# Performance work log

Hardware: AMD Instinct MI355X
Metric: run time of the kernel (lower is better)

The kernel has to match this reference:

```python
import jax, jax.numpy as jnp
import numpy as np

# ----- static layer configuration (mirrors __init__ / _precompute_cg_tensor) -----
NODE_LS = [0, 0, 1, 1]          # node_l_values (multiplicity expressed via repetition; node_multiplicity=1)
EDGE_SH = 1                      # edge_sh_degree
H_LS = NODE_LS + NODE_LS + [0]   # l-values of h = [f_src, f_tgt, d]
H_DIMS = [2 * l + 1 for l in H_LS]
H_OFF = np.concatenate([[0], np.cumsum(H_DIMS)])
A_DIMS = [2 * l + 1 for l in range(EDGE_SH + 1)]
A_OFF = np.concatenate([[0], np.cumsum(A_DIMS)])
O_DIMS = [2 * l + 1 for l in NODE_LS]
O_OFF = np.concatenate([[0], np.cumsum(O_DIMS)])
F_DIM = int(O_OFF[-1])           # 8
A_DIM = int(A_OFF[-1])           # 4
N_NODES, N_EDGES = 100000, 1600000
MLP_DIMS = [2 * len(NODE_LS) + 1, 64, 32, len(NODE_LS)]  # 9 -> 64 -> 32 -> 4

def _levi_civita():
    e = np.zeros((3, 3, 3), np.float32)
    e[0, 1, 2] = e[1, 2, 0] = e[2, 0, 1] = 1.0
    e[0, 2, 1] = e[2, 1, 0] = e[1, 0, 2] = -1.0
    return e

# real SO(3) Clebsch-Gordan tensors (e3nn wigner_3j normalization: full contraction norm 1)
_CG = {
    (0, 0, 0): np.ones((1, 1, 1), np.float32),
    (0, 1, 1): (np.eye(3, dtype=np.float32) / np.sqrt(3.0)).reshape(1, 3, 3),
    (1, 0, 1): (np.eye(3, dtype=np.float32) / np.sqrt(3.0)).reshape(3, 1, 3),
    (1, 1, 0): (np.eye(3, dtype=np.float32) / np.sqrt(3.0)).reshape(3, 3, 1),
    (1, 1, 1): _levi_civita() / np.sqrt(6.0),
}

CONNECTIONS = []  # (h_idx, a_l, out_idx, cg[h,a,o]) -- same enumeration order as the torch loop
for _h_idx, _hl in enumerate(H_LS):
    for _al in range(EDGE_SH + 1):
        for _oi, _ol in enumerate(NODE_LS):
            if abs(_hl - _al) <= _ol <= _hl + _al and (_hl, _al, _ol) in _CG:
                CONNECTIONS.append((_h_idx, _al, _oi, jnp.asarray(_CG[(_hl, _al, _ol)])))


def _invariants(x):
    # s_i = [f_{l=0}, ||f_{l=1}||, ...] per l-slot (multiplicity 1)
    outs = []
    for i, l in enumerate(NODE_LS):
        s, e = int(O_OFF[i]), int(O_OFF[i + 1])
        if l == 0:
            outs.append(x[:, s:e])
        else:
            outs.append(jnp.linalg.norm(x[:, s:e], axis=1, keepdims=True))
    return jnp.concatenate(outs, axis=1)


def setup_inputs() -> dict:
    ks = jax.random.split(jax.random.key(0), 10)
    edge_index = jax.random.randint(ks[0], (2, N_EDGES), 0, N_NODES)
    f = jax.random.normal(ks[1], (N_NODES, F_DIM), jnp.float32)
    d = jax.random.uniform(ks[2], (N_EDGES, 1), jnp.float32)
    a = jax.random.normal(ks[3], (N_EDGES, A_DIM), jnp.float32)
    w1 = jax.random.normal(ks[4], (EDGE_SH + 1,), jnp.float32) * 0.1
    w2 = jax.random.normal(ks[5], (EDGE_SH + 1,), jnp.float32) * 0.1
    W0 = jax.random.normal(ks[6], (MLP_DIMS[0], MLP_DIMS[1]), jnp.float32) / np.sqrt(MLP_DIMS[0])
    b0 = jnp.zeros((MLP_DIMS[1],), jnp.float32)
    W1 = jax.random.normal(ks[7], (MLP_DIMS[1], MLP_DIMS[2]), jnp.float32) / np.sqrt(MLP_DIMS[1])
    b1 = jnp.zeros((MLP_DIMS[2],), jnp.float32)
    W2 = jax.random.normal(ks[8], (MLP_DIMS[2], MLP_DIMS[3]), jnp.float32) / np.sqrt(MLP_DIMS[2])
    b2 = jnp.zeros((MLP_DIMS[3],), jnp.float32)
    return {"edge_index": edge_index, "f": f, "d": d, "a": a, "w1": w1, "w2": w2,
            "W0": W0, "b0": b0, "W1": W1, "b1": b1, "W2": W2, "b2": b2}


def reference(edge_index, f, d, a, w1, w2, W0, b0, W1, b1, W2, b2):
    src, tgt = edge_index[0], edge_index[1]
    n = f.shape[0]
    h = jnp.concatenate([f[src], f[tgt], d], axis=1)  # [E, 17]
    messages = jnp.zeros((h.shape[0], F_DIM), f.dtype)
    for h_idx, a_l, out_idx, cg in CONNECTIONS:
        hs, he = int(H_OFF[h_idx]), int(H_OFF[h_idx + 1])
        as_, ae = int(A_OFF[a_l]), int(A_OFF[a_l + 1])
        os_, oe = int(O_OFF[out_idx]), int(O_OFF[out_idx + 1])
        raw = jnp.einsum('hao,eh,ea->eo', cg, h[:, hs:he], a[:, as_:ae])  # [E, 2*out_l+1]
        msg = jnp.tanh(w2[a_l] * jnp.tanh(w1[a_l] * raw))
        messages = messages.at[:, os_:oe].add(msg)
    agg = jax.ops.segment_sum(messages, tgt, num_segments=n)          # [N, 8]
    dist_sum = jax.ops.segment_sum(d, tgt, num_segments=n)           # [N, 1]
    counts = jax.ops.segment_sum(jnp.ones((h.shape[0],), f.dtype), tgt, num_segments=n)
    avg_d = dist_sum / (counts[:, None] + 1e-8)
    psi_in = jnp.concatenate([_invariants(f), _invariants(agg), avg_d], axis=1)  # [N, 9]
    x = jax.nn.relu(psi_in @ W0 + b0)
    x = jax.nn.relu(x @ W1 + b1)
    gates = jax.nn.sigmoid(x @ W2 + b2)  # [N, 4]
    gate_full = jnp.concatenate(
        [jnp.repeat(gates[:, i:i + 1], O_DIMS[i], axis=1) for i in range(len(NODE_LS))], axis=1)
    return f + gate_full * agg
```

## Files before the change

### kernel.cpp

```cpp
#include <hip/hip_runtime.h>
#include <math.h>

#define IS3 0.57735026918962576f
#define IS6 0.40824829046386302f

#define SHIFT 11
#define BSZ   2048
#define CAP   36864u
#define MQ    4096.0f
#define IMQ   (1.0f/4096.0f)

typedef float v2f __attribute__((ext_vector_type(2)));

__device__ __forceinline__ float fastrcp(float x) { return __builtin_amdgcn_rcpf(x); }
__device__ __forceinline__ v2f mk2(float a, float b) { v2f r; r.x = a; r.y = b; return r; }

__device__ __forceinline__ v2f Tnl2(v2f x, v2f tw1, v2f w2) {
    v2f t = tw1 * x;
    v2f e;
    e.x = __expf(t.x);
    e.y = __expf(t.y);
    v2f ep = e + 1.0f;
    v2f r;
    r.x = fastrcp(ep.x);
    r.y = fastrcp(ep.y);
    v2f u = 1.0f - 2.0f * r;
    v2f z = w2 * u;
    v2f z2 = z * z;
    v2f p = z2 * 0.133333333f - 0.333333333f;
    return z * z2 * p + z;
}

__device__ __forceinline__ int q16(float x) {
    int v = (int)rintf(x * MQ);
    v = v >  32767 ?  32767 : v;
    v = v < -32768 ? -32768 : v;
    return v;
}

__global__ __launch_bounds__(1024, 8) void route_kernel(
    const int* __restrict__ ei, const float* __restrict__ f,
    const float* __restrict__ d, const float* __restrict__ a,
    const float* __restrict__ w1p, const float* __restrict__ w2p,
    unsigned* __restrict__ tails,
    unsigned* __restrict__ qmeta,
    uint2* __restrict__ qmsg,
    int E, int nbuk)
{
    __shared__ unsigned hcnt[64];
    __shared__ unsigned hoff[64];
    int tid = threadIdx.x;
    if (tid < 64) hcnt[tid] = 0;

    int e = blockIdx.x * 1024 + tid;
    bool valid = (e < E);

    float tw10 = 2.0f * w1p[0], tw11 = 2.0f * w1p[1];
    float w20 = w2p[0], w21 = w2p[1];

    int t = 0, s = 0;
    float4 sA = make_float4(0.f,0.f,0.f,0.f), sB = sA, tA = sA, tB = sA, av = sA;
    float de = 0.f;
    if (valid) {
        t = ei[E + e];
        s = ei[e];
        const float4* f4 = (const float4*)f;
        sA = f4[2*s]; sB = f4[2*s+1];
        tA = f4[2*t]; tB = f4[2*t+1];
        de = d[e];
        av = ((const float4*)a)[e];
    }

    __syncthreads();

    unsigned b = 0, lrank = 0;
    if (valid) {
        b = (((unsigned)t) >> SHIFT) & 63u;
        lrank = atomicAdd(&hcnt[b], 1u);
    }
    __syncthreads();

    unsigned basek = 0;
    if (tid < nbuk && hcnt[tid] != 0u)
        basek = atomicAdd(&tails[tid * 64], hcnt[tid]);

    unsigned dq = 0;
    uint2 pk = make_uint2(0u, 0u);
    if (valid) {
        float a0 = av.x, ax = av.y, ay = av.z, az = av.w;
        float axs = ax * IS3, ays = ay * IS3, azs = az * IS3;
        float a03 = a0 * IS3;

        v2f twSX = mk2(tw10, tw11), w2SX = mk2(w20, w21);
        v2f twXY = mk2(tw11, tw11), w2XY = mk2(w21, w21);
        v2f twCX = mk2(tw11, tw10), w2CX = mk2(w21, w20);
        v2f twDD = mk2(tw10, tw10), w2DD = mk2(w20, w20);

        v2f aSX = mk2(a0, axs);
        v2f aYZ = mk2(ays, azs);

        float sc[5] = { sA.x, sA.y, tA.x, tA.y, de };
        float vx[4] = { sA.z, sB.y, tA.z, tB.y };
        float vy[4] = { sA.w, sB.z, tA.w, tB.z };
        float vz[4] = { sB.x, sB.w, tB.x, tB.w };

        v2f mSX = mk2(0.f, 0.f);
        v2f mYZ = mk2(0.f, 0.f);
        float cz6[4];

        #pragma unroll
        for (int i = 0; i < 5; ++i) {
            mSX += Tnl2(sc[i] * aSX, twSX, w2SX);
            mYZ += Tnl2(sc[i] * aYZ, twXY, w2XY);
        }
        #pragma unroll
        for (int i = 0; i < 4; ++i) {
            float dva = vx[i]*ax + vy[i]*ay + vz[i]*az;
            mSX += Tnl2(mk2(dva * IS3, vx[i] * a03), twCX, w2CX);
            mYZ += Tnl2(mk2(vy[i] * a03, vz[i] * a03), twDD, w2DD);
            float cx = vy[i]*az - vz[i]*ay;
            float cy = vz[i]*ax - vx[i]*az;
            float cz = vx[i]*ay - vy[i]*ax;
            v2f exy = Tnl2(mk2(cx * IS6, cy * IS6), twXY, w2XY);
            mSX.y += exy.x;
            mYZ.x += exy.y;
            cz6[i] = cz * IS6;
        }
        v2f g1 = Tnl2(mk2(cz6[0], cz6[1]), twXY, w2XY);
        v2f g2 = Tnl2(mk2(cz6[2], cz6[3]), twXY, w2XY);
        mYZ.y += (g1.x + g1.y) + (g2.x + g2.y);

        unsigned dqi = (unsigned)(de * 2047.0f + 0.5f);
        dq = dqi > 2047u ? 2047u : dqi;
        int qS = q16(mSX.x), qX = q16(mSX.y), qY = q16(mYZ.x), qZ = q16(mYZ.y);
        pk.x = ((unsigned)(unsigned short)qS) | (((unsigned)(unsigned short)qX) << 16);
        pk.y = ((unsigned)(unsigned short)qY) | (((unsigned)(unsigned short)qZ) << 16);
    }

    if (tid < nbuk) hoff[tid] = basek;
    __syncthreads();

    if (valid) {
        unsigned pos = hoff[b] + lrank;
        if (pos < CAP) {
            size_t idx = (size_t)b * CAP + pos;
            qmeta[idx] = (((unsigned)(t & (BSZ - 1))) << 11) | dq;
            qmsg[idx]  = pk;
        }
    }
}

__global__ __launch_bounds__(1024) void bucket_kernel(
    const unsigned* __restrict__ tails, const unsigned* __restrict__ qmeta,
    const uint2* __restrict__ qmsg, unsigned* __restrict__ partial,
    int nbuk, int seg)
{
    __shared__ unsigned long long accSX[BSZ];
    __shared__ unsigned long long accYZ[BSZ];
    __shared__ unsigned accM[BSZ];
    int wg = blockIdx.x;
    int b = wg / seg, sgi = wg % seg;
    for (int i = threadIdx.x; i < BSZ; i += 1024) {
        accSX[i] = 0ull; accYZ[i] = 0ull; accM[i] = 0u;
    }
    __syncthreads();

    unsigned tail = tails[b * 64];
    if (tail > CAP) tail = CAP;
    unsigned lo = (unsigned)(((unsigned long long)tail * sgi) / seg);
    unsigned hi = (unsigned)(((unsigned long long)tail * (sgi + 1)) / seg);
    size_t base = (size_t)b * CAP;

    for (unsigned q = lo + threadIdx.x; q < hi; q += 1024) {
        unsigned meta = qmeta[base + q];
        uint2 m = qmsg[base + q];
        int local = (int)(meta >> 11);
        int qS = (int)(short)(m.x & 0xFFFFu);
        int qX = (int)(short)(m.x >> 16);
        int qY = (int)(short)(m.y & 0xFFFFu);
        int qZ = (int)(short)(m.y >> 16);
        unsigned long long vSX =
            (((unsigned long long)(unsigned)qX) << 32) | (unsigned)(qS + 65536);
        unsigned long long vYZ =
            (((unsigned long long)(unsigned)qZ) << 32) | (unsigned)(qY + 65536);
        atomicAdd(&accSX[local], vSX);
        atomicAdd(&accYZ[local], vYZ);
        atomicAdd(&accM[local], (1u << 20) | (meta & 2047u));
    }
    __syncthreads();

    unsigned* dst = partial + (size_t)wg * (BSZ * 5);
    for (int i = threadIdx.x; i < BSZ; i += 1024) {
        unsigned long long sx = accSX[i], yz = accYZ[i];
        dst[0*BSZ + i] = (unsigned)sx;
        dst[1*BSZ + i] = (unsigned)(sx >> 32);
        dst[2*BSZ + i] = (unsigned)yz;
        dst[3*BSZ + i] = (unsigned)(yz >> 32);
        dst[4*BSZ + i] = accM[i];
    }
}

__global__ __launch_bounds__(512) void mlp_kernel(
    const float* __restrict__ f, const unsigned* __restrict__ partial,
    const float* __restrict__ W0, const float* __restrict__ b0,
    const float* __restrict__ W1, const float* __restrict__ b1,
    const float* __restrict__ W2, const float* __restrict__ b2,
    float* __restrict__ out, int N, int seg)
{
    __shared__ float4 sW0t4[64*3];
    __shared__ float4 sW1v[64*8];
    __shared__ float4 sW2v[32];
    __shared__ float  sb0[64];
    __shared__ float4 sb1v[8];
    __shared__ float4 sb2v[1];

    int tid = threadIdx.x;
    float* w0t = (float*)sW0t4;
    for (int idx = tid; idx < 576; idx += 512) {
        int k = idx >> 6, i = idx & 63;
        w0t[i * 12 + k] = W0[idx];
    }
    if (tid < 192) {
        int i = tid / 3, k = 9 + tid % 3;
        w0t[i * 12 + k] = 0.f;
    }
    { float* p = (float*)sW1v; for (int idx = tid; idx < 2048; idx += 512) p[idx] = W1[idx]; }
    { float* p = (float*)sW2v; if (tid < 128) p[tid] = W2[tid]; }
    if (tid < 64) sb0[tid] = b0[tid];
    { float* p = (float*)sb1v; if (tid < 32) p[tid] = b1[tid]; }
    { float* p = (float*)sb2v; if (tid < 4)  p[tid] = b2[tid]; }
    __syncthreads();

    int n = blockIdx.x * 512 + tid;
    if (n >= N) return;

    int b = n >> SHIFT;
    int local = n & (BSZ - 1);
    int S = 0, X = 0, Y = 0, Z = 0, cnt = 0, dqs = 0;
    for (int s2 = 0; s2 < seg; ++s2) {
        const unsigned* p = partial + ((size_t)(b * seg + s2)) * (BSZ * 5);
        unsigned m4 = p[4*BSZ + local];
        int c = (int)(m4 >> 20);
        S += (int)p[0*BSZ + local] - (c << 16);
        X += (int)p[1*BSZ + local];
        Y += (int)p[2*BSZ + local] - (c << 16);
        Z += (int)p[3*BSZ + local];
        dqs += (int)(m4 & 0xFFFFFu);
        cnt += c;
    }
    float aS = (float)S * IMQ, ax = (float)X * IMQ;
    float ay = (float)Y * IMQ, az = (float)Z * IMQ;
    float cf = (float)cnt;
    float dsum = (float)dqs * (1.0f / 2047.0f);

    float4 fA = ((const float4*)f)[2*n];
    float4 fB = ((const float4*)f)[2*n+1];

    float nrm1 = sqrtf(fA.z*fA.z + fA.w*fA.w + fB.x*fB.x);
    float nrm2 = sqrtf(fB.y*fB.y + fB.z*fB.z + fB.w*fB.w);
    float nv   = sqrtf(ax*ax + ay*ay + az*az);
    float avgd = dsum * fastrcp(cf + 1e-8f);
    float4 p0 = make_float4(fA.x, fA.y, nrm1, nrm2);
    float4 p1 = make_float4(aS, aS, nv, nv);
    float4 p2 = make_float4(avgd, 0.f, 0.f, 0.f);

    float x1s[32];
    #pragma unroll
    for (int j = 0; j < 8; ++j) {
        float4 bv = sb1v[j];
        x1s[4*j+0] = bv.x; x1s[4*j+1] = bv.y; x1s[4*j+2] = bv.z; x1s[4*j+3] = bv.w;
    }
    #pragma unroll
    for (int i = 0; i < 64; ++i) {
        float4 r0 = sW0t4[i*3+0], r1 = sW0t4[i*3+1], r2 = sW0t4[i*3+2];
        float acc = sb0[i]
            + r0.x*p0.x + r0.y*p0.y + r0.z*p0.z + r0.w*p0.w
            + r1.x*p1.x + r1.y*p1.y + r1.z*p1.z + r1.w*p1.w
            + r2.x*p2.x;
        acc = fmaxf(acc, 0.f);
        #pragma unroll
        for (int j = 0; j < 8; ++j) {
            float4 wv = sW1v[i*8+j];
            x1s[4*j+0] += acc * wv.x;
            x1s[4*j+1] += acc * wv.y;
            x1s[4*j+2] += acc * wv.z;
            x1s[4*j+3] += acc * wv.w;
        }
    }
    #pragma unroll
    for (int j = 0; j < 32; ++j) x1s[j] = fmaxf(x1s[j], 0.f);

    float4 gb = sb2v[0];
    float g0 = gb.x, g1 = gb.y, g2 = gb.z, g3 = gb.w;
    #pragma unroll
    for (int i = 0; i < 32; ++i) {
        float4 wv = sW2v[i];
        g0 += x1s[i] * wv.x;
        g1 += x1s[i] * wv.y;
        g2 += x1s[i] * wv.z;
        g3 += x1s[i] * wv.w;
    }
    g0 = fastrcp(1.0f + __expf(-g0));
    g1 = fastrcp(1.0f + __expf(-g1));
    g2 = fastrcp(1.0f + __expf(-g2));
    g3 = fastrcp(1.0f + __expf(-g3));

    float* o = out + (size_t)8*n;
    o[0] = fA.x + g0*aS;
    o[1] = fA.y + g1*aS;
    o[2] = fA.z + g2*ax;
    o[3] = fA.w + g2*ay;
    o[4] = fB.x + g2*az;
    o[5] = fB.y + g3*ax;
    o[6] = fB.z + g3*ay;
    o[7] = fB.w + g3*az;
}

extern "C" void kernel_launch(void* const* d_in, const int* in_sizes, int n_in,
                              void* d_out, int out_size, void* d_ws, size_t ws_size,
                              hipStream_t stream) {
    const int*   ei = (const int*)d_in[0];
    const float* f  = (const float*)d_in[1];
    const float* d  = (const float*)d_in[2];
    const float* a  = (const float*)d_in[3];
    const float* w1 = (const float*)d_in[4];
    const float* w2 = (const float*)d_in[5];
    const float* W0 = (const float*)d_in[6];
    const float* b0 = (const float*)d_in[7];
    const float* W1 = (const float*)d_in[8];
    const float* b1 = (const float*)d_in[9];
    const float* W2 = (const float*)d_in[10];
    const float* b2 = (const float*)d_in[11];
    int E = in_sizes[0] / 2;
    int N = in_sizes[1] / 8;
    int nbuk = (N + BSZ - 1) >> SHIFT;

    size_t qn = (size_t)nbuk * CAP;
    size_t fixed = qn * 12 + (size_t)nbuk * 64 * 4;
    size_t per_seg = (size_t)nbuk * BSZ * 5 * 4;
    int segmax = nbuk > 0 ? (512 / nbuk) : 6;
    if (segmax < 1) segmax = 1;
    int seg = 6;
    if (ws_size > fixed + per_seg) {
        size_t m = (ws_size - fixed) / per_seg;
        seg = (int)(m < (size_t)segmax ? m : (size_t)segmax);
        if (seg < 1) seg = 1;
    }

    char* w = (char*)d_ws;
    uint2*    qmsg    = (uint2*)w;
    unsigned* qmeta   = (unsigned*)(w + qn * 8);
    unsigned* partial = (unsigned*)(w + qn * 12);
    unsigned* tails   = (unsigned*)(w + qn * 12 + (size_t)seg * per_seg);

    hipMemsetAsync(tails, 0, (size_t)nbuk * 64 * sizeof(unsigned), stream);

    int EB = (E + 1023) / 1024;
    route_kernel <<<dim3(EB), dim3(1024), 0, stream>>>(
        ei, f, d, a, w1, w2, tails, qmeta, qmsg, E, nbuk);
    bucket_kernel<<<dim3(nbuk * seg), dim3(1024), 0, stream>>>(
        tails, qmeta, qmsg, partial, nbuk, seg);
    mlp_kernel   <<<dim3((N + 511) / 512), dim3(512), 0, stream>>>(
        f, partial, W0, b0, W1, b1, W2, b2, (float*)d_out, N, seg);
}
```

Before: 175.0 us.

## Pre-pack MLP weights once and process two nodes per thread from global

Adds a one-block prep kernel that writes W0 (transposed and padded), W1, W2 and the biases into a packed workspace buffer. The MLP kernel then reads these uniform weights straight from global/scalar cache instead of staging them in shared memory with a barrier in every block. Each 64-thread block now handles two nodes per lane, so every weight load is reused across two rows. This costs one extra launch and doubles register pressure for the 32-wide hidden accumulators, which may lower occupancy.

```diff
diff --git a/kernel.cpp b/kernel.cpp
--- a/kernel.cpp
+++ b/kernel.cpp
@@ -9,6 +9,7 @@
 #define CAP   36864u
 #define MQ    4096.0f
 #define IMQ   (1.0f/4096.0f)
+#define WPAD  16384
 
 typedef float v2f __attribute__((ext_vector_type(2)));
 
@@ -36,6 +37,24 @@
     v = v >  32767 ?  32767 : v;
     v = v < -32768 ? -32768 : v;
     return v;
+}
+
+__global__ __launch_bounds__(1024) void prep_kernel(
+    const float* __restrict__ W0, const float* __restrict__ b0,
+    const float* __restrict__ W1, const float* __restrict__ b1,
+    const float* __restrict__ W2, const float* __restrict__ b2,
+    float* __restrict__ wp)
+{
+    int tid = threadIdx.x;
+    if (tid < 768) {
+        int i = tid / 12, k = tid % 12;
+        wp[tid] = (k < 9) ? W0[k * 64 + i] : 0.f;
+    }
+    for (int idx = tid; idx < 2048; idx += 1024) wp[768 + idx] = W1[idx];
+    if (tid < 128) wp[2816 + tid] = W2[tid];
+    if (tid < 64)  wp[2944 + tid] = b0[tid];
+    if (tid < 32)  wp[3008 + tid] = b1[tid];
+    if (tid < 4)   wp[3040 + tid] = b2[tid];
 }
 
 __global__ __launch_bounds__(1024, 8) void route_kernel(
@@ -200,120 +219,163 @@
     }
 }
 
-__global__ __launch_bounds__(512) void mlp_kernel(
+__global__ __launch_bounds__(64) void mlp_kernel(
     const float* __restrict__ f, const unsigned* __restrict__ partial,
-    const float* __restrict__ W0, const float* __restrict__ b0,
-    const float* __restrict__ W1, const float* __restrict__ b1,
-    const float* __restrict__ W2, const float* __restrict__ b2,
-    float* __restrict__ out, int N, int seg)
+    const float* __restrict__ wp, float* __restrict__ out, int N, int seg)
 {
-    __shared__ float4 sW0t4[64*3];
-    __shared__ float4 sW1v[64*8];
-    __shared__ float4 sW2v[32];
-    __shared__ float  sb0[64];
-    __shared__ float4 sb1v[8];
-    __shared__ float4 sb2v[1];
-
-    int tid = threadIdx.x;
-    float* w0t = (float*)sW0t4;
-    for (int idx = tid; idx < 576; idx += 512) {
-        int k = idx >> 6, i = idx & 63;
-        w0t[i * 12 + k] = W0[idx];
-    }
-    if (tid < 192) {
-        int i = tid / 3, k = 9 + tid % 3;
-        w0t[i * 12 + k] = 0.f;
-    }
-    { float* p = (float*)sW1v; for (int idx = tid; idx < 2048; idx += 512) p[idx] = W1[idx]; }
-    { float* p = (float*)sW2v; if (tid < 128) p[tid] = W2[tid]; }
-    if (tid < 64) sb0[tid] = b0[tid];
-    { float* p = (float*)sb1v; if (tid < 32) p[tid] = b1[tid]; }
-    { float* p = (float*)sb2v; if (tid < 4)  p[tid] = b2[tid]; }
-    __syncthreads();
-
-    int n = blockIdx.x * 512 + tid;
-    if (n >= N) return;
-
-    int b = n >> SHIFT;
-    int local = n & (BSZ - 1);
-    int S = 0, X = 0, Y = 0, Z = 0, cnt = 0, dqs = 0;
+    int lane = threadIdx.x;
+    int n0 = blockIdx.x * 128 + lane;
+    int n1 = n0 + 64;
+    if (n0 >= N) return;
+    bool vB = (n1 < N);
+
+    const float4* w0t4 = (const float4*)(wp);
+    const float4* w1v  = (const float4*)(wp + 768);
+    const float4* w2v  = (const float4*)(wp + 2816);
+    const float*  pb0  = wp + 2944;
+    const float4* b1v  = (const float4*)(wp + 3008);
+    const float4* b2v  = (const float4*)(wp + 3040);
+
+    int bA = n0 >> SHIFT, lA = n0 & (BSZ - 1);
+    int SA=0, XA=0, YA=0, ZA=0, cntA=0, dqsA=0;
     for (int s2 = 0; s2 < seg; ++s2) {
-        const unsigned* p = partial + ((size_t)(b * seg + s2)) * (BSZ * 5);
-        unsigned m4 = p[4*BSZ + local];
+        const unsigned* p = partial + ((size_t)(bA * seg + s2)) * (BSZ * 5);
+        unsigned m4 = p[4*BSZ + lA];
         int c = (int)(m4 >> 20);
-        S += (int)p[0*BSZ + local] - (c << 16);
-        X += (int)p[1*BSZ + local];
-        Y += (int)p[2*BSZ + local] - (c << 16);
-        Z += (int)p[3*BSZ + local];
-        dqs += (int)(m4 & 0xFFFFFu);
-        cnt += c;
-    }
-    float aS = (float)S * IMQ, ax = (float)X * IMQ;
-    float ay = (float)Y * IMQ, az = (float)Z * IMQ;
-    float cf = (float)cnt;
-    float dsum = (float)dqs * (1.0f / 2047.0f);
-
-    float4 fA = ((const float4*)f)[2*n];
-    float4 fB = ((const float4*)f)[2*n+1];
-
-    float nrm1 = sqrtf(fA.z*fA.z + fA.w*fA.w + fB.x*fB.x);
-    float nrm2 = sqrtf(fB.y*fB.y + fB.z*fB.z + fB.w*fB.w);
-    float nv   = sqrtf(ax*ax + ay*ay + az*az);
-    float avgd = dsum * fastrcp(cf + 1e-8f);
-    float4 p0 = make_float4(fA.x, fA.y, nrm1, nrm2);
-    float4 p1 = make_float4(aS, aS, nv, nv);
-    float4 p2 = make_float4(avgd, 0.f, 0.f, 0.f);
-
-    float x1s[32];
+        SA += (int)p[0*BSZ + lA] - (c << 16);
+        XA += (int)p[1*BSZ + lA];
+        YA += (int)p[2*BSZ + lA] - (c << 16);
+        ZA += (int)p[3*BSZ + lA];
+        dqsA += (int)(m4 & 0xFFFFFu);
+        cntA += c;
+    }
+    int bB = vB ? (n1 >> SHIFT) : 0, lB = vB ? (n1 & (BSZ - 1)) : 0;
+    int SB=0, XB=0, YB=0, ZB=0, cntB=0, dqsB=0;
+    if (vB) {
+        for (int s2 = 0; s2 < seg; ++s2) {
+            const unsigned* p = partial + ((size_t)(bB * seg + s2)) * (BSZ * 5);
+            unsigned m4 = p[4*BSZ + lB];
+            int c = (int)(m4 >> 20);
+            SB += (int)p[0*BSZ + lB] - (c << 16);
+            XB += (int)p[1*BSZ + lB];
+            YB += (int)p[2*BSZ + lB] - (c << 16);
+            ZB += (int)p[3*BSZ + lB];
+            dqsB += (int)(m4 & 0xFFFFFu);
+            cntB += c;
+        }
+    }
+
+    float aSA = (float)SA * IMQ, axA = (float)XA * IMQ;
+    float ayA = (float)YA * IMQ, azA = (float)ZA * IMQ;
+    float dsumA = (float)dqsA * (1.0f / 2047.0f);
+    float aSB = (float)SB * IMQ, axB = (float)XB * IMQ;
+    float ayB = (float)YB * IMQ, azB = (float)ZB * IMQ;
+    float dsumB = (float)dqsB * (1.0f / 2047.0f);
+
+    const float4* f4 = (const float4*)f;
+    float4 fA0 = f4[2*n0], fB0 = f4[2*n0+1];
+    float4 fA1 = make_float4(0.f,0.f,0.f,0.f), fB1 = fA1;
+    if (vB) { fA1 = f4[2*n1]; fB1 = f4[2*n1+1]; }
+
+    float nrm1A = sqrtf(fA0.z*fA0.z + fA0.w*fA0.w + fB0.x*fB0.x);
+    float nrm2A = sqrtf(fB0.y*fB0.y + fB0.z*fB0.z + fB0.w*fB0.w);
+    float nvA   = sqrtf(axA*axA + ayA*ayA + azA*azA);
+    float avgdA = dsumA * fastrcp((float)cntA + 1e-8f);
+    float4 p0A = make_float4(fA0.x, fA0.y, nrm1A, nrm2A);
+    float4 p1A = make_float4(aSA, aSA, nvA, nvA);
+
+    float nrm1B = sqrtf(fA1.z*fA1.z + fA1.w*fA1.w + fB1.x*fB1.x);
+    float nrm2B = sqrtf(fB1.y*fB1.y + fB1.z*fB1.z + fB1.w*fB1.w);
+    float nvB   = sqrtf(axB*axB + ayB*ayB + azB*azB);
+    float avgdB = dsumB * fastrcp((float)cntB + 1e-8f);
+    float4 p0B = make_float4(fA1.x, fA1.y, nrm1B, nrm2B);
+    float4 p1B = make_float4(aSB, aSB, nvB, nvB);
+
+    float x1A[32], x1B[32];
     #pragma unroll
     for (int j = 0; j < 8; ++j) {
-        float4 bv = sb1v[j];
-        x1s[4*j+0] = bv.x; x1s[4*j+1] = bv.y; x1s[4*j+2] = bv.z; x1s[4*j+3] = bv.w;
-    }
-    #pragma unroll
+        float4 bv = b1v[j];
+        x1A[4*j+0] = bv.x; x1A[4*j+1] = bv.y; x1A[4*j+2] = bv.z; x1A[4*j+3] = bv.w;
+        x1B[4*j+0] = bv.x; x1B[4*j+1] = bv.y; x1B[4*j+2] = bv.z; x1B[4*j+3] = bv.w;
+    }
+    #pragma unroll 8
     for (int i = 0; i < 64; ++i) {
-        float4 r0 = sW0t4[i*3+0], r1 = sW0t4[i*3+1], r2 = sW0t4[i*3+2];
-        float acc = sb0[i]
-            + r0.x*p0.x + r0.y*p0.y + r0.z*p0.z + r0.w*p0.w
-            + r1.x*p1.x + r1.y*p1.y + r1.z*p1.z + r1.w*p1.w
-            + r2.x*p2.x;
-        acc = fmaxf(acc, 0.f);
+        float4 r0 = w0t4[i*3+0], r1 = w0t4[i*3+1], r2 = w0t4[i*3+2];
+        float bb = pb0[i];
+        float accA = bb
+            + r0.x*p0A.x + r0.y*p0A.y + r0.z*p0A.z + r0.w*p0A.w
+            + r1.x*p1A.x + r1.y*p1A.y + r1.z*p1A.z + r1.w*p1A.w
+            + r2.x*avgdA;
+        float accB = bb
+            + r0.x*p0B.x + r0.y*p0B.y + r0.z*p0B.z + r0.w*p0B.w
+            + r1.x*p1B.x + r1.y*p1B.y + r1.z*p1B.z + r1.w*p1B.w
+            + r2.x*avgdB;
+        accA = fmaxf(accA, 0.f);
+        accB = fmaxf(accB, 0.f);
         #pragma unroll
         for (int j = 0; j < 8; ++j) {
-            float4 wv = sW1v[i*8+j];
-            x1s[4*j+0] += acc * wv.x;
-            x1s[4*j+1] += acc * wv.y;
-            x1s[4*j+2] += acc * wv.z;
-            x1s[4*j+3] += acc * wv.w;
+            float4 wv = w1v[i*8+j];
+            x1A[4*j+0] += accA * wv.x;
+            x1A[4*j+1] += accA * wv.y;
+            x1A[4*j+2] += accA * wv.z;
+            x1A[4*j+3] += accA * wv.w;
+            x1B[4*j+0] += accB * wv.x;
+            x1B[4*j+1] += accB * wv.y;
+            x1B[4*j+2] += accB * wv.z;
+            x1B[4*j+3] += accB * wv.w;
         }
     }
     #pragma unroll
-    for (int j = 0; j < 32; ++j) x1s[j] = fmaxf(x1s[j], 0.f);
-
-    float4 gb = sb2v[0];
-    float g0 = gb.x, g1 = gb.y, g2 = gb.z, g3 = gb.w;
+    for (int j = 0; j < 32; ++j) {
+        x1A[j] = fmaxf(x1A[j], 0.f);
+        x1B[j] = fmaxf(x1B[j], 0.f);
+    }
+
+    float4 gb = b2v[0];
+    float g0A = gb.x, g1A = gb.y, g2A = gb.z, g3A = gb.w;
+    float g0B = gb.x, g1B = gb.y, g2B = gb.z, g3B = gb.w;
     #pragma unroll
     for (int i = 0; i < 32; ++i) {
-        float4 wv = sW2v[i];
-        g0 += x1s[i] * wv.x;
-        g1 += x1s[i] * wv.y;
-        g2 += x1s[i] * wv.z;
-        g3 += x1s[i] * wv.w;
-    }
-    g0 = fastrcp(1.0f + __expf(-g0));
-    g1 = fastrcp(1.0f + __expf(-g1));
-    g2 = fastrcp(1.0f + __expf(-g2));
-    g3 = fastrcp(1.0f + __expf(-g3));
-
-    float* o = out + (size_t)8*n;
-    o[0] = fA.x + g0*aS;
-    o[1] = fA.y + g1*aS;
-    o[2] = fA.z + g2*ax;
-    o[3] = fA.w + g2*ay;
-    o[4] = fB.x + g2*az;
-    o[5] = fB.y + g3*ax;
-    o[6] = fB.z + g3*ay;
-    o[7] = fB.w + g3*az;
+        float4 wv = w2v[i];
+        g0A += x1A[i] * wv.x;
+        g1A += x1A[i] * wv.y;
+        g2A += x1A[i] * wv.z;
+        g3A += x1A[i] * wv.w;
+        g0B += x1B[i] * wv.x;
+        g1B += x1B[i] * wv.y;
+        g2B += x1B[i] * wv.z;
+        g3B += x1B[i] * wv.w;
+    }
+    g0A = fastrcp(1.0f + __expf(-g0A));
+    g1A = fastrcp(1.0f + __expf(-g1A));
+    g2A = fastrcp(1.0f + __expf(-g2A));
+    g3A = fastrcp(1.0f + __expf(-g3A));
+
+    float* oA = out + (size_t)8*n0;
+    oA[0] = fA0.x + g0A*aSA;
+    oA[1] = fA0.y + g1A*aSA;
+    oA[2] = fA0.z + g2A*axA;
+    oA[3] = fA0.w + g2A*ayA;
+    oA[4] = fB0.x + g2A*azA;
+    oA[5] = fB0.y + g3A*axA;
+    oA[6] = fB0.z + g3A*ayA;
+    oA[7] = fB0.w + g3A*azA;
+
+    if (vB) {
+        g0B = fastrcp(1.0f + __expf(-g0B));
+        g1B = fastrcp(1.0f + __expf(-g1B));
+        g2B = fastrcp(1.0f + __expf(-g2B));
+        g3B = fastrcp(1.0f + __expf(-g3B));
+        float* oB = out + (size_t)8*n1;
+        oB[0] = fA1.x + g0B*aSB;
+        oB[1] = fA1.y + g1B*aSB;
+        oB[2] = fA1.z + g2B*axB;
+        oB[3] = fA1.w + g2B*ayB;
+        oB[4] = fB1.x + g2B*azB;
+        oB[5] = fB1.y + g3B*axB;
+        oB[6] = fB1.z + g3B*ayB;
+        oB[7] = fB1.w + g3B*azB;
+    }
 }
 
 extern "C" void kernel_launch(void* const* d_in, const int* in_sizes, int n_in,
@@ -336,7 +398,7 @@
     int nbuk = (N + BSZ - 1) >> SHIFT;
 
     size_t qn = (size_t)nbuk * CAP;
-    size_t fixed = qn * 12 + (size_t)nbuk * 64 * 4;
+    size_t fixed = (size_t)WPAD + qn * 12 + (size_t)nbuk * 64 * 4;
     size_t per_seg = (size_t)nbuk * BSZ * 5 * 4;
     int segmax = nbuk > 0 ? (512 / nbuk) : 6;
     if (segmax < 1) segmax = 1;
@@ -348,18 +410,21 @@
     }
 
     char* w = (char*)d_ws;
-    uint2*    qmsg    = (uint2*)w;
-    unsigned* qmeta   = (unsigned*)(w + qn * 8);
-    unsigned* partial = (unsigned*)(w + qn * 12);
-    unsigned* tails   = (unsigned*)(w + qn * 12 + (size_t)seg * per_seg);
+    float*    wp      = (float*)w;
+    uint2*    qmsg    = (uint2*)(w + WPAD);
+    unsigned* qmeta   = (unsigned*)(w + WPAD + qn * 8);
+    unsigned* partial = (unsigned*)(w + WPAD + qn * 12);
+    unsigned* tails   = (unsigned*)(w + WPAD + qn * 12 + (size_t)seg * per_seg);
 
     hipMemsetAsync(tails, 0, (size_t)nbuk * 64 * sizeof(unsigned), stream);
+
+    prep_kernel<<<dim3(1), dim3(1024), 0, stream>>>(W0, b0, W1, b1, W2, b2, wp);
 
     int EB = (E + 1023) / 1024;
     route_kernel <<<dim3(EB), dim3(1024), 0, stream>>>(
         ei, f, d, a, w1, w2, tails, qmeta, qmsg, E, nbuk);
     bucket_kernel<<<dim3(nbuk * seg), dim3(1024), 0, stream>>>(
         tails, qmeta, qmsg, partial, nbuk, seg);
-    mlp_kernel   <<<dim3((N + 511) / 512), dim3(512), 0, stream>>>(
-        f, partial, W0, b0, W1, b1, W2, b2, (float*)d_out, N, seg);
-}
+    mlp_kernel   <<<dim3((N + 127) / 128), dim3(64), 0, stream>>>(
+        f, partial, wp, (float*)d_out, N, seg);
+}
```

New measurement: 211.3 us. +20.7%, slower.

## Split MLP across 8 lanes per node with shuffle reductions

Applied to the files above, without the earlier changes.

The MLP/finalize kernel now assigns 8 threads per node instead of one. The lanes split the segment-partial reads and the 64 hidden units of layer 0, then combine partial sums with xor shuffles. Weights are read straight from global memory (cached) instead of being staged in LDS, which removes the per-block weight load and barrier. The segment count is a template parameter, and a generic fallback handles other values. The aim is less per-thread serial work and more parallelism over 100k nodes, at the cost of many shuffle reductions (32 outputs times 3 steps).

```diff
diff --git a/kernel.cpp b/kernel.cpp
--- a/kernel.cpp
+++ b/kernel.cpp
@@ -200,38 +200,149 @@
     }
 }
 
-__global__ __launch_bounds__(512) void mlp_kernel(
+template<int SEGC>
+__global__ __launch_bounds__(256, 4) void mlp_kernel(
+    const float* __restrict__ f, const unsigned* __restrict__ partial,
+    const float* __restrict__ W0, const float* __restrict__ b0,
+    const float* __restrict__ W1, const float* __restrict__ b1,
+    const float* __restrict__ W2, const float* __restrict__ b2,
+    float* __restrict__ out, int N)
+{
+    int tid = threadIdx.x;
+    int s   = tid & 7;
+    int n   = blockIdx.x * 32 + (tid >> 3);
+    bool vn = (n < N);
+    int nc  = vn ? n : (N - 1);
+
+    int b = nc >> SHIFT, local = nc & (BSZ - 1);
+    int S = 0, X = 0, Y = 0, Z = 0, cnt = 0, dqs = 0;
+    for (int s2 = s; s2 < SEGC; s2 += 8) {
+        const unsigned* p = partial + ((size_t)(b * SEGC + s2)) * (BSZ * 5);
+        unsigned m4 = p[4*BSZ + local];
+        S   += (int)p[0*BSZ + local];
+        X   += (int)p[1*BSZ + local];
+        Y   += (int)p[2*BSZ + local];
+        Z   += (int)p[3*BSZ + local];
+        dqs += (int)(m4 & 0xFFFFFu);
+        cnt += (int)(m4 >> 20);
+    }
+    #pragma unroll
+    for (int r = 1; r <= 4; r <<= 1) {
+        S   += __shfl_xor(S, r);
+        X   += __shfl_xor(X, r);
+        Y   += __shfl_xor(Y, r);
+        Z   += __shfl_xor(Z, r);
+        cnt += __shfl_xor(cnt, r);
+        dqs += __shfl_xor(dqs, r);
+    }
+    S -= cnt << 16;
+    Y -= cnt << 16;
+
+    float aS = (float)S * IMQ, ax = (float)X * IMQ;
+    float ay = (float)Y * IMQ, az = (float)Z * IMQ;
+    float dsum = (float)dqs * (1.0f / 2047.0f);
+
+    const float4* f4 = (const float4*)f;
+    float4 fA = f4[2*nc], fB = f4[2*nc+1];
+
+    float nrm1 = sqrtf(fA.z*fA.z + fA.w*fA.w + fB.x*fB.x);
+    float nrm2 = sqrtf(fB.y*fB.y + fB.z*fB.z + fB.w*fB.w);
+    float nv   = sqrtf(ax*ax + ay*ay + az*az);
+    float avgd = dsum * fastrcp((float)cnt + 1e-8f);
+    float pk9[9] = { fA.x, fA.y, nrm1, nrm2, aS, aS, nv, nv, avgd };
+
+    const float4* W0v = (const float4*)W0;
+    const float4* b0v = (const float4*)b0;
+    float h[8];
+    {
+        float4 ba = b0v[2*s], bb = b0v[2*s+1];
+        h[0]=ba.x; h[1]=ba.y; h[2]=ba.z; h[3]=ba.w;
+        h[4]=bb.x; h[5]=bb.y; h[6]=bb.z; h[7]=bb.w;
+    }
+    #pragma unroll
+    for (int k = 0; k < 9; ++k) {
+        float4 wa = W0v[k*16 + 2*s];
+        float4 wb = W0v[k*16 + 2*s + 1];
+        float pv = pk9[k];
+        h[0] += pv*wa.x; h[1] += pv*wa.y; h[2] += pv*wa.z; h[3] += pv*wa.w;
+        h[4] += pv*wb.x; h[5] += pv*wb.y; h[6] += pv*wb.z; h[7] += pv*wb.w;
+    }
+    #pragma unroll
+    for (int u = 0; u < 8; ++u) h[u] = fmaxf(h[u], 0.f);
+
+    const float4* W1v = (const float4*)W1;
+    float x1p[32];
+    #pragma unroll
+    for (int m = 0; m < 32; ++m) x1p[m] = 0.f;
+    #pragma unroll
+    for (int u = 0; u < 8; ++u) {
+        int i = 8*s + u;
+        float hv = h[u];
+        #pragma unroll
+        for (int mq = 0; mq < 8; ++mq) {
+            float4 wv = W1v[i*8 + mq];
+            x1p[4*mq+0] += hv * wv.x;
+            x1p[4*mq+1] += hv * wv.y;
+            x1p[4*mq+2] += hv * wv.z;
+            x1p[4*mq+3] += hv * wv.w;
+        }
+    }
+    #pragma unroll
+    for (int m = 0; m < 32; ++m) {
+        float v = x1p[m];
+        v += __shfl_xor(v, 1);
+        v += __shfl_xor(v, 2);
+        v += __shfl_xor(v, 4);
+        x1p[m] = v;
+    }
+    const float4* b1v4 = (const float4*)b1;
+    #pragma unroll
+    for (int mq = 0; mq < 8; ++mq) {
+        float4 bv = b1v4[mq];
+        x1p[4*mq+0] = fmaxf(x1p[4*mq+0] + bv.x, 0.f);
+        x1p[4*mq+1] = fmaxf(x1p[4*mq+1] + bv.y, 0.f);
+        x1p[4*mq+2] = fmaxf(x1p[4*mq+2] + bv.z, 0.f);
+        x1p[4*mq+3] = fmaxf(x1p[4*mq+3] + bv.w, 0.f);
+    }
+
+    const float4* W2v = (const float4*)W2;
+    float4 gb = *(const float4*)b2;
+    float g0 = gb.x, g1 = gb.y, g2 = gb.z, g3 = gb.w;
+    #pragma unroll
+    for (int m = 0; m < 32; ++m) {
+        float4 wv = W2v[m];
+        g0 += x1p[m] * wv.x;
+        g1 += x1p[m] * wv.y;
+        g2 += x1p[m] * wv.z;
+        g3 += x1p[m] * wv.w;
+    }
+    if (!vn) return;
+    g0 = fastrcp(1.0f + __expf(-g0));
+    g1 = fastrcp(1.0f + __expf(-g1));
+    g2 = fastrcp(1.0f + __expf(-g2));
+    g3 = fastrcp(1.0f + __expf(-g3));
+
+    float t01 = (s == 0) ? fA.x : fA.y;
+    float t23 = (s == 2) ? fA.z : fA.w;
+    float t45 = (s == 4) ? fB.x : fB.y;
+    float t67 = (s == 6) ? fB.z : fB.w;
+    float tlo = (s < 2) ? t01 : t23;
+    float thi = (s < 6) ? t45 : t67;
+    float fv  = (s < 4) ? tlo : thi;
+    float gv  = (s == 0) ? g0 : (s == 1) ? g1 : (s < 5) ? g2 : g3;
+    float av  = (s < 2) ? aS : ((s == 2 || s == 5) ? ax
+              : ((s == 3 || s == 6) ? ay : az));
+    out[(size_t)8*n + s] = fv + gv * av;
+}
+
+__global__ __launch_bounds__(256) void mlp_kernel_gen(
     const float* __restrict__ f, const unsigned* __restrict__ partial,
     const float* __restrict__ W0, const float* __restrict__ b0,
     const float* __restrict__ W1, const float* __restrict__ b1,
     const float* __restrict__ W2, const float* __restrict__ b2,
     float* __restrict__ out, int N, int seg)
 {
-    __shared__ float4 sW0t4[64*3];
-    __shared__ float4 sW1v[64*8];
-    __shared__ float4 sW2v[32];
-    __shared__ float  sb0[64];
-    __shared__ float4 sb1v[8];
-    __shared__ float4 sb2v[1];
-
-    int tid = threadIdx.x;
-    float* w0t = (float*)sW0t4;
-    for (int idx = tid; idx < 576; idx += 512) {
-        int k = idx >> 6, i = idx & 63;
-        w0t[i * 12 + k] = W0[idx];
-    }
-    if (tid < 192) {
-        int i = tid / 3, k = 9 + tid % 3;
-        w0t[i * 12 + k] = 0.f;
-    }
-    { float* p = (float*)sW1v; for (int idx = tid; idx < 2048; idx += 512) p[idx] = W1[idx]; }
-    { float* p = (float*)sW2v; if (tid < 128) p[tid] = W2[tid]; }
-    if (tid < 64) sb0[tid] = b0[tid];
-    { float* p = (float*)sb1v; if (tid < 32) p[tid] = b1[tid]; }
-    { float* p = (float*)sb2v; if (tid < 4)  p[tid] = b2[tid]; }
-    __syncthreads();
-
-    int n = blockIdx.x * 512 + tid;
+    int n = blockIdx.x * 256 + threadIdx.x;
     if (n >= N) return;
 
     int b = n >> SHIFT;
@@ -250,7 +361,6 @@
     }
     float aS = (float)S * IMQ, ax = (float)X * IMQ;
     float ay = (float)Y * IMQ, az = (float)Z * IMQ;
-    float cf = (float)cnt;
     float dsum = (float)dqs * (1.0f / 2047.0f);
 
     float4 fA = ((const float4*)f)[2*n];
@@ -259,46 +369,30 @@
     float nrm1 = sqrtf(fA.z*fA.z + fA.w*fA.w + fB.x*fB.x);
     float nrm2 = sqrtf(fB.y*fB.y + fB.z*fB.z + fB.w*fB.w);
     float nv   = sqrtf(ax*ax + ay*ay + az*az);
-    float avgd = dsum * fastrcp(cf + 1e-8f);
-    float4 p0 = make_float4(fA.x, fA.y, nrm1, nrm2);
-    float4 p1 = make_float4(aS, aS, nv, nv);
-    float4 p2 = make_float4(avgd, 0.f, 0.f, 0.f);
+    float avgd = dsum * fastrcp((float)cnt + 1e-8f);
+    float pk9[9] = { fA.x, fA.y, nrm1, nrm2, aS, aS, nv, nv, avgd };
 
     float x1s[32];
     #pragma unroll
-    for (int j = 0; j < 8; ++j) {
-        float4 bv = sb1v[j];
-        x1s[4*j+0] = bv.x; x1s[4*j+1] = bv.y; x1s[4*j+2] = bv.z; x1s[4*j+3] = bv.w;
-    }
-    #pragma unroll
+    for (int j = 0; j < 32; ++j) x1s[j] = b1[j];
     for (int i = 0; i < 64; ++i) {
-        float4 r0 = sW0t4[i*3+0], r1 = sW0t4[i*3+1], r2 = sW0t4[i*3+2];
-        float acc = sb0[i]
-            + r0.x*p0.x + r0.y*p0.y + r0.z*p0.z + r0.w*p0.w
-            + r1.x*p1.x + r1.y*p1.y + r1.z*p1.z + r1.w*p1.w
-            + r2.x*p2.x;
+        float acc = b0[i];
+        #pragma unroll
+        for (int k = 0; k < 9; ++k) acc += pk9[k] * W0[k*64 + i];
         acc = fmaxf(acc, 0.f);
         #pragma unroll
-        for (int j = 0; j < 8; ++j) {
-            float4 wv = sW1v[i*8+j];
-            x1s[4*j+0] += acc * wv.x;
-            x1s[4*j+1] += acc * wv.y;
-            x1s[4*j+2] += acc * wv.z;
-            x1s[4*j+3] += acc * wv.w;
-        }
+        for (int j = 0; j < 32; ++j) x1s[j] += acc * W1[i*32 + j];
     }
     #pragma unroll
     for (int j = 0; j < 32; ++j) x1s[j] = fmaxf(x1s[j], 0.f);
 
-    float4 gb = sb2v[0];
-    float g0 = gb.x, g1 = gb.y, g2 = gb.z, g3 = gb.w;
+    float g0 = b2[0], g1 = b2[1], g2 = b2[2], g3 = b2[3];
     #pragma unroll
     for (int i = 0; i < 32; ++i) {
-        float4 wv = sW2v[i];
-        g0 += x1s[i] * wv.x;
-        g1 += x1s[i] * wv.y;
-        g2 += x1s[i] * wv.z;
-        g3 += x1s[i] * wv.w;
+        g0 += x1s[i] * W2[i*4+0];
+        g1 += x1s[i] * W2[i*4+1];
+        g2 += x1s[i] * W2[i*4+2];
+        g3 += x1s[i] * W2[i*4+3];
     }
     g0 = fastrcp(1.0f + __expf(-g0));
     g1 = fastrcp(1.0f + __expf(-g1));
@@ -360,6 +454,21 @@
         ei, f, d, a, w1, w2, tails, qmeta, qmsg, E, nbuk);
     bucket_kernel<<<dim3(nbuk * seg), dim3(1024), 0, stream>>>(
         tails, qmeta, qmsg, partial, nbuk, seg);
-    mlp_kernel   <<<dim3((N + 511) / 512), dim3(512), 0, stream>>>(
-        f, partial, W0, b0, W1, b1, W2, b2, (float*)d_out, N, seg);
-}
+
+    dim3 mg((N + 31) / 32), mb(256);
+    switch (seg) {
+      case 1:  mlp_kernel<1> <<<mg, mb, 0, stream>>>(f, partial, W0,b0,W1,b1,W2,b2, (float*)d_out, N); break;
+      case 2:  mlp_kernel<2> <<<mg, mb, 0, stream>>>(f, partial, W0,b0,W1,b1,W2,b2, (float*)d_out, N); break;
+      case 3:  mlp_kernel<3> <<<mg, mb, 0, stream>>>(f, partial, W0,b0,W1,b1,W2,b2, (float*)d_out, N); break;
+      case 4:  mlp_kernel<4> <<<mg, mb, 0, stream>>>(f, partial, W0,b0,W1,b1,W2,b2, (float*)d_out, N); break;
+      case 5:  mlp_kernel<5> <<<mg, mb, 0, stream>>>(f, partial, W0,b0,W1,b1,W2,b2, (float*)d_out, N); break;
+      case 6:  mlp_kernel<6> <<<mg, mb, 0, stream>>>(f, partial, W0,b0,W1,b1,W2,b2, (float*)d_out, N); break;
+      case 7:  mlp_kernel<7> <<<mg, mb, 0, stream>>>(f, partial, W0,b0,W1,b1,W2,b2, (float*)d_out, N); break;
+      case 8:  mlp_kernel<8> <<<mg, mb, 0, stream>>>(f, partial, W0,b0,W1,b1,W2,b2, (float*)d_out, N); break;
+      case 9:  mlp_kernel<9> <<<mg, mb, 0, stream>>>(f, partial, W0,b0,W1,b1,W2,b2, (float*)d_out, N); break;
+      case 10: mlp_kernel<10><<<mg, mb, 0, stream>>>(f, partial, W0,b0,W1,b1,W2,b2, (float*)d_out, N); break;
+      default:
+        mlp_kernel_gen<<<dim3((N + 255) / 256), dim3(256), 0, stream>>>(
+            f, partial, W0,b0,W1,b1,W2,b2, (float*)d_out, N, seg);
+    }
+}
```

New measurement: 255.5 us. +46.0%, slower.
